# Kernel optimization log

Measured on AMD Instinct MI355X. Metric: run time of the kernel, lower is better.

The kernel has to match this reference:

```python
import math
import jax, jax.numpy as jnp
import numpy as np

B, S, D, H = 4, 2048, 1024, 16
HD = D // H  # head_dim = 64

def setup_inputs() -> dict:
    key = jax.random.key(0)
    k1, k2, k3 = jax.random.split(key, 3)
    scale_in = 1.0 / math.sqrt(D)
    return {
        "x": jax.random.normal(k1, (B, S, D), dtype=jnp.float32),
        "W_in": jax.random.normal(k2, (D, 3 * D), dtype=jnp.float32) * scale_in,
        "b_in": jnp.zeros((3 * D,), dtype=jnp.float32),
        "W_out": jax.random.normal(k3, (D, D), dtype=jnp.float32) * scale_in,
        "b_out": jnp.zeros((D,), dtype=jnp.float32),
    }

def reference(x, W_in, b_in, W_out, b_out):
    b, s, d = x.shape
    proj = x @ W_in + b_in                       # [B,S,3D]
    # torch.chunk order: keys, queries, values
    k, q, v = jnp.split(proj, 3, axis=-1)
    def heads(t):
        return t.reshape(b, s, H, HD).transpose(0, 2, 1, 3)  # [B,H,S,HD]
    q, k, v = heads(q), heads(k), heads(v)
    scores = jnp.einsum('bhqd,bhkd->bhqk', q, k) / math.sqrt(HD)
    causal = jnp.tril(jnp.ones((s, s), dtype=bool))
    scores = jnp.where(causal[None, None], scores, -jnp.inf)
    attn = jax.nn.softmax(scores, axis=-1)        # dropout p=0 (eval)
    out = jnp.einsum('bhqk,bhkd->bhqd', attn, v)  # [B,H,S,HD]
    out = out.transpose(0, 2, 1, 3).reshape(b, s, d)
    return out @ W_out + b_out
```

## Files before the change

kernel.cpp:

```cpp
#include <hip/hip_runtime.h>
#include <hip/hip_bf16.h>


typedef float f32x4 __attribute__((ext_vector_type(4)));
typedef __bf16 bf16x8 __attribute__((ext_vector_type(8)));

__device__ __forceinline__ ushort f2bf(float f) {
    uint u = __builtin_bit_cast(uint, f);
    u += 0x7fff + ((u >> 16) & 1);
    return (ushort)(u >> 16);
}

#define GLL16(g, lp)                                                            \
    __builtin_amdgcn_global_load_lds(                                           \
        (const __attribute__((address_space(1))) uint*)(const void*)(g),        \
        (__attribute__((address_space(3))) uint*)(void*)(lp), 16, 0, 0)

#define SWZ(row, chunk) ((row) * 64 + ((((chunk) ^ ((row) & 7))) * 8))

__global__ __launch_bounds__(256) void cvt_f32_bf16(const float* __restrict__ in,
                                                    ushort* __restrict__ out, int n) {
    int i = (blockIdx.x * 256 + threadIdx.x) * 8;
    if (i >= n) return;
    float4 a = *(const float4*)&in[i];
    float4 b = *(const float4*)&in[i + 4];
    uint4 o;
    o.x = (uint)f2bf(a.x) | ((uint)f2bf(a.y) << 16);
    o.y = (uint)f2bf(a.z) | ((uint)f2bf(a.w) << 16);
    o.z = (uint)f2bf(b.x) | ((uint)f2bf(b.y) << 16);
    o.w = (uint)f2bf(b.z) | ((uint)f2bf(b.w) << 16);
    *(uint4*)&out[i] = o;
}

__global__ __launch_bounds__(256) void trans_cvt(const float* __restrict__ in,
                                                 ushort* __restrict__ out, int R, int C) {
    __shared__ float t[32][33];
    int tx = threadIdx.x & 31, ty = threadIdx.x >> 5;
    int c0 = blockIdx.x * 32, r0 = blockIdx.y * 32;
#pragma unroll
    for (int i = 0; i < 4; i++)
        t[ty + i * 8][tx] = in[(size_t)(r0 + ty + i * 8) * C + c0 + tx];
    __syncthreads();
#pragma unroll
    for (int i = 0; i < 4; i++)
        out[(size_t)(c0 + ty + i * 8) * R + r0 + tx] = f2bf(t[tx][ty + i * 8]);
}

__global__ __launch_bounds__(256) void vtrans(const ushort* __restrict__ proj,
                                              ushort* __restrict__ vT) {
    __shared__ ushort t[128][34];
    int tid = threadIdx.x;
    int bx = blockIdx.x;
    int st = bx & 15, hdt = (bx >> 4) & 1, bh = bx >> 5;
    int b = bh >> 4, h = bh & 15;
    const ushort* src = proj + (size_t)(b * 2048 + st * 128) * 3072 + 2048 + h * 64 + hdt * 32;
    int hdx = tid & 31, sy = tid >> 5;
#pragma unroll
    for (int i = 0; i < 16; i++)
        t[sy + i * 8][hdx] = src[(size_t)(sy + i * 8) * 3072 + hdx];
    __syncthreads();
    int tx = tid & 127, ty = tid >> 7;
    ushort* dst = vT + ((size_t)bh * 64 + hdt * 32) * 2048 + st * 128;
#pragma unroll
    for (int i = 0; i < 16; i++)
        dst[(size_t)(ty + i * 2) * 2048 + tx] = t[tx][ty + i * 2];
}

template <int OUTF32>
__global__ __launch_bounds__(256) void gemm_bt(const ushort* __restrict__ A,
                                               const ushort* __restrict__ Bt,
                                               const float* __restrict__ bias,
                                               void* __restrict__ Cv,
                                               int M, int N, int K) {
    __shared__ ushort As[128 * 32];
    __shared__ ushort Bs[128 * 32];
    int tid = threadIdx.x;
    int w = tid >> 6, l = tid & 63;
    int l16 = l & 15, lq = l >> 4;
    int tn = N >> 7;
    int bx = blockIdx.x;
    int row0 = (bx / tn) * 128, col0 = (bx % tn) * 128;
    int wr = w >> 1, wc = w & 1;

    f32x4 acc[4][4];
#pragma unroll
    for (int m = 0; m < 4; m++)
#pragma unroll
        for (int n = 0; n < 4; n++) acc[m][n] = (f32x4){0.f, 0.f, 0.f, 0.f};

    int c0 = tid, c1 = tid + 256;
    const ushort* ag0 = A + (size_t)(row0 + (c0 >> 2)) * K + (c0 & 3) * 8;
    const ushort* ag1 = A + (size_t)(row0 + (c1 >> 2)) * K + (c1 & 3) * 8;
    const ushort* bg0 = Bt + (size_t)(col0 + (c0 >> 2)) * K + (c0 & 3) * 8;
    const ushort* bg1 = Bt + (size_t)(col0 + (c1 >> 2)) * K + (c1 & 3) * 8;
    ushort* la0 = As + w * 512;
    ushort* la1 = As + 2048 + w * 512;
    ushort* lb0 = Bs + w * 512;
    ushort* lb1 = Bs + 2048 + w * 512;

    for (int k0 = 0; k0 < K; k0 += 32) {
        GLL16(ag0 + k0, la0);
        GLL16(ag1 + k0, la1);
        GLL16(bg0 + k0, lb0);
        GLL16(bg1 + k0, lb1);
        __syncthreads();
        bf16x8 af[4], bfv[4];
#pragma unroll
        for (int m = 0; m < 4; m++)
            af[m] = *(const bf16x8*)&As[(wr * 64 + m * 16 + l16) * 32 + lq * 8];
#pragma unroll
        for (int n = 0; n < 4; n++)
            bfv[n] = *(const bf16x8*)&Bs[(wc * 64 + n * 16 + l16) * 32 + lq * 8];
#pragma unroll
        for (int m = 0; m < 4; m++)
#pragma unroll
            for (int n = 0; n < 4; n++)
                acc[m][n] = __builtin_amdgcn_mfma_f32_16x16x32_bf16(af[m], bfv[n], acc[m][n], 0, 0, 0);
        __syncthreads();
    }

#pragma unroll
    for (int m = 0; m < 4; m++) {
        int row = row0 + wr * 64 + m * 16 + lq * 4;
#pragma unroll
        for (int n = 0; n < 4; n++) {
            int col = col0 + wc * 64 + n * 16 + l16;
            float bv = bias[col];
#pragma unroll
            for (int r = 0; r < 4; r++) {
                float v = acc[m][n][r] + bv;
                if (OUTF32)
                    ((float*)Cv)[(size_t)(row + r) * N + col] = v;
                else
                    ((ushort*)Cv)[(size_t)(row + r) * N + col] = f2bf(v);
            }
        }
    }
}

__global__ __launch_bounds__(256) void attn_kern(const ushort* __restrict__ proj,
                                                 const ushort* __restrict__ vT,
                                                 ushort* __restrict__ attno) {
    constexpr int S = 2048, TD = 3072;
    __shared__ ushort Ks[2][64 * 64];
    __shared__ ushort Vs[2][64 * 64];
    __shared__ ushort Ps[4][16 * 64];

    int tid = threadIdx.x;
    int w = tid >> 6, l = tid & 63;
    int l16 = l & 15, lq = l >> 4;
    int bx = blockIdx.x;
    int pi = bx & 15, bh = bx >> 4;
    int b = bh >> 4, h = bh & 15;
    int qbA = pi * 64, qbB = (31 - pi) * 64;
    int nA = pi + 1;
    int ntot = 33;
    const size_t base = (size_t)b * S * TD;

    bf16x8 aqA0, aqA1, aqB0, aqB1;
    {
        const ushort* qpA = proj + base + (size_t)(qbA + w * 16 + l16) * TD + 1024 + h * 64 + lq * 8;
        aqA0 = *(const bf16x8*)(qpA);
        aqA1 = *(const bf16x8*)(qpA + 32);
        const ushort* qpB = proj + base + (size_t)(qbB + w * 16 + l16) * TD + 1024 + h * 64 + lq * 8;
        aqB0 = *(const bf16x8*)(qpB);
        aqB1 = *(const bf16x8*)(qpB + 32);
    }

    int c0 = tid, c1 = tid + 256;
    int r0 = c0 >> 3, ch0 = (c0 & 7) ^ (r0 & 7);
    int r1 = c1 >> 3, ch1 = (c1 & 7) ^ (r1 & 7);
    const ushort* kgb = proj + base + h * 64;
    const ushort* vgb = vT + (size_t)bh * 64 * 2048;

#define STAGE(bufi, j)                                                              \
    {                                                                               \
        int kb_ = (((j) < nA) ? (j) : ((j) - nA)) * 64;                             \
        GLL16(kgb + (size_t)(kb_ + r0) * TD + ch0 * 8, &Ks[bufi][w * 512]);         \
        GLL16(kgb + (size_t)(kb_ + r1) * TD + ch1 * 8, &Ks[bufi][2048 + w * 512]);  \
        GLL16(vgb + (size_t)r0 * 2048 + kb_ + ch0 * 8, &Vs[bufi][w * 512]);         \
        GLL16(vgb + (size_t)r1 * 2048 + kb_ + ch1 * 8, &Vs[bufi][2048 + w * 512]);  \
    }

    float m_r[4], lsum[4];
    f32x4 o[4];
#pragma unroll
    for (int r = 0; r < 4; r++) { m_r[r] = -1e30f; lsum[r] = 0.f; }
#pragma unroll
    for (int n = 0; n < 4; n++) o[n] = (f32x4){0.f, 0.f, 0.f, 0.f};

    bf16x8 aq0 = aqA0, aq1 = aqA1;
    int qrow_d = qbA + w * 16 + lq * 4;

    int buf = 0;
    STAGE(0, 0);

    for (int j = 0; j < ntot; j++) {
        if (j + 1 < ntot) {
            STAGE(buf ^ 1, j + 1);
            asm volatile("s_waitcnt vmcnt(4)" ::: "memory");
        } else {
            asm volatile("s_waitcnt vmcnt(0)" ::: "memory");
        }
        __builtin_amdgcn_sched_barrier(0);
        __builtin_amdgcn_s_barrier();

        if (j == nA) {
#pragma unroll
            for (int r = 0; r < 4; r++) {
                float inv = 1.0f / lsum[r];
                size_t ob = ((size_t)b * S + qrow_d + r) * 1024 + h * 64;
#pragma unroll
                for (int n = 0; n < 4; n++)
                    attno[ob + n * 16 + l16] = f2bf(o[n][r] * inv);
            }
#pragma unroll
            for (int r = 0; r < 4; r++) { m_r[r] = -1e30f; lsum[r] = 0.f; }
#pragma unroll
            for (int n = 0; n < 4; n++) o[n] = (f32x4){0.f, 0.f, 0.f, 0.f};
            aq0 = aqB0; aq1 = aqB1;
            qrow_d = qbB + w * 16 + lq * 4;
        }
        int kb = ((j < nA) ? j : (j - nA)) * 64;

        f32x4 sacc[4];
#pragma unroll
        for (int n = 0; n < 4; n++) sacc[n] = (f32x4){0.f, 0.f, 0.f, 0.f};
#pragma unroll
        for (int n = 0; n < 4; n++) {
            bf16x8 bk0 = *(const bf16x8*)&Ks[buf][SWZ(n * 16 + l16, lq)];
            bf16x8 bk1 = *(const bf16x8*)&Ks[buf][SWZ(n * 16 + l16, 4 + lq)];
            sacc[n] = __builtin_amdgcn_mfma_f32_16x16x32_bf16(aq0, bk0, sacc[n], 0, 0, 0);
            sacc[n] = __builtin_amdgcn_mfma_f32_16x16x32_bf16(aq1, bk1, sacc[n], 0, 0, 0);
        }

        float p[4][4];
#pragma unroll
        for (int n = 0; n < 4; n++) {
            int col = kb + n * 16 + l16;
#pragma unroll
            for (int r = 0; r < 4; r++) {
                float sc = sacc[n][r] * 0.125f;
                if (col > qrow_d + r) sc = -1e30f;
                p[n][r] = sc;
            }
        }
#pragma unroll
        for (int r = 0; r < 4; r++) {
            float mx = fmaxf(fmaxf(p[0][r], p[1][r]), fmaxf(p[2][r], p[3][r]));
#pragma unroll
            for (int mk = 1; mk < 16; mk <<= 1) mx = fmaxf(mx, __shfl_xor(mx, mk));
            float mnew = fmaxf(m_r[r], mx);
            float scale = __expf(m_r[r] - mnew);
            m_r[r] = mnew;
            float rs = 0.f;
#pragma unroll
            for (int n = 0; n < 4; n++) {
                float e = __expf(p[n][r] - mnew);
                p[n][r] = e;
                rs += e;
            }
#pragma unroll
            for (int mk = 1; mk < 16; mk <<= 1) rs += __shfl_xor(rs, mk);
            lsum[r] = lsum[r] * scale + rs;
#pragma unroll
            for (int n = 0; n < 4; n++) o[n][r] *= scale;
        }

#pragma unroll
        for (int n = 0; n < 4; n++) {
            int chunkbase = n * 2 + (l16 >> 3);
            int cl = l16 & 7;
#pragma unroll
            for (int r = 0; r < 4; r++) {
                int prow = lq * 4 + r;
                Ps[w][prow * 64 + ((chunkbase ^ (prow & 7)) * 8) + cl] = f2bf(p[n][r]);
            }
        }

        bf16x8 pa0 = *(const bf16x8*)&Ps[w][SWZ(l16, lq)];
        bf16x8 pa1 = *(const bf16x8*)&Ps[w][SWZ(l16, 4 + lq)];
#pragma unroll
        for (int n = 0; n < 4; n++) {
            bf16x8 bv0 = *(const bf16x8*)&Vs[buf][SWZ(n * 16 + l16, lq)];
            bf16x8 bv1 = *(const bf16x8*)&Vs[buf][SWZ(n * 16 + l16, 4 + lq)];
            o[n] = __builtin_amdgcn_mfma_f32_16x16x32_bf16(pa0, bv0, o[n], 0, 0, 0);
            o[n] = __builtin_amdgcn_mfma_f32_16x16x32_bf16(pa1, bv1, o[n], 0, 0, 0);
        }
        __builtin_amdgcn_s_barrier();
        buf ^= 1;
    }

#pragma unroll
    for (int r = 0; r < 4; r++) {
        float inv = 1.0f / lsum[r];
        size_t ob = ((size_t)b * S + qrow_d + r) * 1024 + h * 64;
#pragma unroll
        for (int n = 0; n < 4; n++)
            attno[ob + n * 16 + l16] = f2bf(o[n][r] * inv);
    }
#undef STAGE
}

extern "C" void kernel_launch(void* const* d_in, const int* in_sizes, int n_in,
                              void* d_out, int out_size, void* d_ws, size_t ws_size,
                              hipStream_t stream) {
    const float* x     = (const float*)d_in[0];
    const float* W_in  = (const float*)d_in[1];
    const float* b_in  = (const float*)d_in[2];
    const float* W_out = (const float*)d_in[3];
    const float* b_out = (const float*)d_in[4];
    float* out = (float*)d_out;
    char* ws = (char*)d_ws;

    ushort* xb    = (ushort*)(ws);
    ushort* vT    = (ushort*)(ws);
    ushort* w1t   = (ushort*)(ws + (size_t)16 * 1024 * 1024);
    ushort* w2t   = (ushort*)(ws + (size_t)22 * 1024 * 1024);
    ushort* proj  = (ushort*)(ws + (size_t)24 * 1024 * 1024);
    ushort* attno = (ushort*)(ws + (size_t)72 * 1024 * 1024);

    cvt_f32_bf16<<<4096, 256, 0, stream>>>(x, xb, 8192 * 1024);
    trans_cvt<<<dim3(96, 32), 256, 0, stream>>>(W_in, w1t, 1024, 3072);
    trans_cvt<<<dim3(32, 32), 256, 0, stream>>>(W_out, w2t, 1024, 1024);
    gemm_bt<0><<<64 * 24, 256, 0, stream>>>(xb, w1t, b_in, proj, 8192, 3072, 1024);
    vtrans<<<2048, 256, 0, stream>>>(proj, vT);
    attn_kern<<<1024, 256, 0, stream>>>(proj, vT, attno);
    gemm_bt<1><<<64 * 8, 256, 0, stream>>>(attno, w2t, b_out, out, 8192, 1024, 1024);
}
```

Measured before the change: 341.2 us.

## Double-buffer GEMM LDS loads, remap blocks by XCD, add lazy softmax rescale

The GEMM now double-buffers its LDS tiles. It issues the next k-slice's global_load_lds before computing on the current one, and uses vmcnt waits plus raw barriers in place of full __syncthreads. Block indices are permuted so consecutive tiles land on the same XCD (chiplet), which should improve L2 reuse. In attention, the online softmax skips the max update and the O rescale whenever every row's new max is within 8 of the running max. That trades a wave-wide vote for fewer exps and multiplies, at some risk of reduced fp32 headroom.

```diff
diff --git a/kernel.cpp b/kernel.cpp
--- a/kernel.cpp
+++ b/kernel.cpp
@@ -72,14 +72,15 @@
                                                const float* __restrict__ bias,
                                                void* __restrict__ Cv,
                                                int M, int N, int K) {
-    __shared__ ushort As[128 * 32];
-    __shared__ ushort Bs[128 * 32];
+    __shared__ ushort As[2][128 * 32];
+    __shared__ ushort Bs[2][128 * 32];
     int tid = threadIdx.x;
     int w = tid >> 6, l = tid & 63;
     int l16 = l & 15, lq = l >> 4;
     int tn = N >> 7;
-    int bx = blockIdx.x;
-    int row0 = (bx / tn) * 128, col0 = (bx % tn) * 128;
+    int cpx = gridDim.x >> 3;
+    int wg = (blockIdx.x & 7) * cpx + (blockIdx.x >> 3);
+    int row0 = (wg / tn) * 128, col0 = (wg % tn) * 128;
     int wr = w >> 1, wc = w & 1;
 
     f32x4 acc[4][4];
@@ -93,31 +94,42 @@
     const ushort* ag1 = A + (size_t)(row0 + (c1 >> 2)) * K + (c1 & 3) * 8;
     const ushort* bg0 = Bt + (size_t)(col0 + (c0 >> 2)) * K + (c0 & 3) * 8;
     const ushort* bg1 = Bt + (size_t)(col0 + (c1 >> 2)) * K + (c1 & 3) * 8;
-    ushort* la0 = As + w * 512;
-    ushort* la1 = As + 2048 + w * 512;
-    ushort* lb0 = Bs + w * 512;
-    ushort* lb1 = Bs + 2048 + w * 512;
-
+
+#define GSTAGE(bufi, kk)                                  \
+    {                                                     \
+        GLL16(ag0 + (kk), &As[bufi][w * 512]);            \
+        GLL16(ag1 + (kk), &As[bufi][2048 + w * 512]);     \
+        GLL16(bg0 + (kk), &Bs[bufi][w * 512]);            \
+        GLL16(bg1 + (kk), &Bs[bufi][2048 + w * 512]);     \
+    }
+
+    int buf = 0;
+    GSTAGE(0, 0);
     for (int k0 = 0; k0 < K; k0 += 32) {
-        GLL16(ag0 + k0, la0);
-        GLL16(ag1 + k0, la1);
-        GLL16(bg0 + k0, lb0);
-        GLL16(bg1 + k0, lb1);
-        __syncthreads();
+        if (k0 + 32 < K) {
+            GSTAGE(buf ^ 1, k0 + 32);
+            asm volatile("s_waitcnt vmcnt(4)" ::: "memory");
+        } else {
+            asm volatile("s_waitcnt vmcnt(0)" ::: "memory");
+        }
+        __builtin_amdgcn_sched_barrier(0);
+        __builtin_amdgcn_s_barrier();
         bf16x8 af[4], bfv[4];
 #pragma unroll
         for (int m = 0; m < 4; m++)
-            af[m] = *(const bf16x8*)&As[(wr * 64 + m * 16 + l16) * 32 + lq * 8];
+            af[m] = *(const bf16x8*)&As[buf][(wr * 64 + m * 16 + l16) * 32 + lq * 8];
 #pragma unroll
         for (int n = 0; n < 4; n++)
-            bfv[n] = *(const bf16x8*)&Bs[(wc * 64 + n * 16 + l16) * 32 + lq * 8];
+            bfv[n] = *(const bf16x8*)&Bs[buf][(wc * 64 + n * 16 + l16) * 32 + lq * 8];
 #pragma unroll
         for (int m = 0; m < 4; m++)
 #pragma unroll
             for (int n = 0; n < 4; n++)
                 acc[m][n] = __builtin_amdgcn_mfma_f32_16x16x32_bf16(af[m], bfv[n], acc[m][n], 0, 0, 0);
-        __syncthreads();
-    }
+        __builtin_amdgcn_s_barrier();
+        buf ^= 1;
+    }
+#undef GSTAGE
 
 #pragma unroll
     for (int m = 0; m < 4; m++) {
@@ -245,26 +257,50 @@
                 p[n][r] = sc;
             }
         }
+
+        float mx[4];
 #pragma unroll
         for (int r = 0; r < 4; r++) {
-            float mx = fmaxf(fmaxf(p[0][r], p[1][r]), fmaxf(p[2][r], p[3][r]));
-#pragma unroll
-            for (int mk = 1; mk < 16; mk <<= 1) mx = fmaxf(mx, __shfl_xor(mx, mk));
-            float mnew = fmaxf(m_r[r], mx);
-            float scale = __expf(m_r[r] - mnew);
-            m_r[r] = mnew;
-            float rs = 0.f;
-#pragma unroll
-            for (int n = 0; n < 4; n++) {
-                float e = __expf(p[n][r] - mnew);
-                p[n][r] = e;
-                rs += e;
-            }
-#pragma unroll
-            for (int mk = 1; mk < 16; mk <<= 1) rs += __shfl_xor(rs, mk);
-            lsum[r] = lsum[r] * scale + rs;
-#pragma unroll
-            for (int n = 0; n < 4; n++) o[n][r] *= scale;
+            float v = fmaxf(fmaxf(p[0][r], p[1][r]), fmaxf(p[2][r], p[3][r]));
+#pragma unroll
+            for (int mk = 1; mk < 16; mk <<= 1) v = fmaxf(v, __shfl_xor(v, mk));
+            mx[r] = v;
+        }
+        bool small = (mx[0] <= m_r[0] + 8.f) && (mx[1] <= m_r[1] + 8.f) &&
+                     (mx[2] <= m_r[2] + 8.f) && (mx[3] <= m_r[3] + 8.f);
+        if (__all(small)) {
+#pragma unroll
+            for (int r = 0; r < 4; r++) {
+                float rs = 0.f;
+#pragma unroll
+                for (int n = 0; n < 4; n++) {
+                    float e = __expf(p[n][r] - m_r[r]);
+                    p[n][r] = e;
+                    rs += e;
+                }
+#pragma unroll
+                for (int mk = 1; mk < 16; mk <<= 1) rs += __shfl_xor(rs, mk);
+                lsum[r] += rs;
+            }
+        } else {
+#pragma unroll
+            for (int r = 0; r < 4; r++) {
+                float mnew = fmaxf(m_r[r], mx[r]);
+                float scale = __expf(m_r[r] - mnew);
+                m_r[r] = mnew;
+                float rs = 0.f;
+#pragma unroll
+                for (int n = 0; n < 4; n++) {
+                    float e = __expf(p[n][r] - mnew);
+                    p[n][r] = e;
+                    rs += e;
+                }
+#pragma unroll
+                for (int mk = 1; mk < 16; mk <<= 1) rs += __shfl_xor(rs, mk);
+                lsum[r] = lsum[r] * scale + rs;
+#pragma unroll
+                for (int n = 0; n < 4; n++) o[n][r] *= scale;
+            }
         }
 
 #pragma unroll
```

Measured after the change: 342.7 us. No clear change (+0.4%).
